# Performance work log

Measured on AMD Instinct MI355X. Metric: run time of the kernel, lower is better.

The kernel has to match this reference:

```python
import jax, jax.numpy as jnp
import numpy as np

N_NODES = 50000
N_EDGES = 800000
IN_DIM = 128
HEADS = 4
OUT_DIM = 32
NEG_SLOPE = 0.2


def setup_inputs() -> dict:
    key = jax.random.key(0)
    k_x, k_e, k_w, k_as, k_ad = jax.random.split(key, 5)
    x = jax.random.normal(k_x, (N_NODES, IN_DIM), dtype=jnp.float32)
    edge_index = jax.random.randint(k_e, (2, N_EDGES), 0, N_NODES, dtype=jnp.int32)
    # Linear(in_dim, heads*out_dim, bias=False): store as [in_dim, heads*out_dim]
    W = jax.random.normal(k_w, (IN_DIM, HEADS * OUT_DIM), dtype=jnp.float32) * 0.05
    a_src = jax.random.normal(k_as, (HEADS, OUT_DIM), dtype=jnp.float32) * 0.01
    a_dst = jax.random.normal(k_ad, (HEADS, OUT_DIM), dtype=jnp.float32) * 0.01
    return {"x": x, "edge_index": edge_index, "W": W, "a_src": a_src, "a_dst": a_dst}


def reference(x, edge_index, W, a_src, a_dst):
    N = x.shape[0]
    H, D = a_src.shape
    src, dst = edge_index[0], edge_index[1]
    h = (x @ W).reshape(N, H, D)                      # [N, H, D]
    h_src = h[src]                                    # [E, H, D] gather
    h_dst = h[dst]                                    # [E, H, D] gather
    e = jnp.einsum('ehd,hd->eh', h_src, a_src) + jnp.einsum('ehd,hd->eh', h_dst, a_dst)
    e = jax.nn.leaky_relu(e, NEG_SLOPE)               # [E, H]
    # segment softmax over dst, per head (vectorized across heads)
    m = jax.ops.segment_max(e, dst, num_segments=N)   # [N, H]
    exp = jnp.exp(e - m[dst])                         # [E, H]
    s = jax.ops.segment_sum(exp, dst, num_segments=N) # [N, H]
    alpha = exp / (s[dst] + 1e-12)                    # [E, H]
    # dropout p=0.0 -> identity
    out = jax.ops.segment_sum(alpha[:, :, None] * h_src, dst, num_segments=N)  # [N, H, D]
    return out.mean(axis=1)                           # [N, D]
```

## Files before the change

### kernel.cpp

```cpp
#include <hip/hip_runtime.h>
#include <hip/hip_bf16.h>

#define IN_DIM 128
#define HEADS 4
#define ODIM 32
#define HD (HEADS * ODIM)
#define NEG_SLOPE 0.2f

#define GM 64
#define LDK 136
#define ACCW 132

#define BIN_SHIFT 4
#define BIN_NODES 16
#define BINCAP 512
#define MAXBINS 4096
#define KE 16

#define SMEM_BYTES 52224

typedef unsigned short ushortT;
typedef __attribute__((ext_vector_type(8))) short bf16x8;
typedef __attribute__((ext_vector_type(4))) float f32x4;

static __device__ __forceinline__ ushortT f2bf(float f) {
    __hip_bfloat16 b = __float2bfloat16(f);
    return *reinterpret_cast<ushortT*>(&b);
}
static __device__ __forceinline__ float hsel(float4 v, int head) {
    return (head == 0) ? v.x : (head == 1) ? v.y : (head == 2) ? v.z : v.w;
}
static __device__ __forceinline__ float i8f(unsigned int p, int sh) {
    return (float)((int)(p << (24 - sh)) >> 24);
}

__global__ void __launch_bounds__(256) k_wconv_zero(
    const float* __restrict__ W, ushortT* __restrict__ Wt_g,
    int* __restrict__ bin_cursor, int nbins)
{
    const int idx = blockIdx.x * 256 + threadIdx.x;
    const int c = idx >> 7, k = idx & 127;
    Wt_g[c * 128 + k] = f2bf(W[k * HD + c]);
    if (idx < nbins) bin_cursor[idx] = 0;
}

__global__ void __launch_bounds__(256) k_mega(
    const float* __restrict__ x, const ushortT* __restrict__ Wt_g,
    const float* __restrict__ a_src, const float* __restrict__ a_dst,
    const int* __restrict__ src, const int* __restrict__ dst,
    unsigned char* __restrict__ h8, float* __restrict__ scales,
    float* __restrict__ s_src, float* __restrict__ s_dst,
    int* __restrict__ bin_cursor, int* __restrict__ bin_buf,
    int N, int E, int nbins, int nBinBlocks)
{
    __shared__ __align__(16) char smem[SMEM_BYTES];
    const int t = threadIdx.x;

    if ((int)blockIdx.x < nBinBlocks) {
        int* lcnt = reinterpret_cast<int*>(smem);
        int* lcur = lcnt + MAXBINS;
        for (int i = t; i < nbins; i += 256) lcnt[i] = 0;
        __syncthreads();

        const int base_e = blockIdx.x * (256 * KE);
        int b_[KE]; int p_[KE];
#pragma unroll
        for (int k = 0; k < KE; ++k) {
            const int e = base_e + k * 256 + t;
            if (e < E) {
                const int d = dst[e];
                const int s = src[e];
                b_[k] = d >> BIN_SHIFT;
                p_[k] = ((d & (BIN_NODES - 1)) << 16) | s;
                atomicAdd(&lcnt[b_[k]], 1);
            } else {
                b_[k] = -1;
            }
        }
        __syncthreads();
        for (int i = t; i < nbins; i += 256) {
            const int c = lcnt[i];
            lcur[i] = (c > 0) ? atomicAdd(&bin_cursor[i], c) : 0;
        }
        __syncthreads();
#pragma unroll
        for (int k = 0; k < KE; ++k) {
            if (b_[k] >= 0) {
                const int pos = atomicAdd(&lcur[b_[k]], 1);
                if (pos < BINCAP) bin_buf[b_[k] * BINCAP + pos] = p_[k];
            }
        }
        return;
    }

    ushortT* Xs = reinterpret_cast<ushortT*>(smem);
    ushortT* Wt = Xs + GM * LDK;

    const int n0 = ((int)blockIdx.x - nBinBlocks) * GM;

    {
#pragma unroll
        for (int it = 0; it < 8; ++it) {
            const int o = it * 2048 + t * 8;
            *reinterpret_cast<uint4*>(&Wt[(o >> 7) * LDK + (o & 127)]) =
                *reinterpret_cast<const uint4*>(&Wt_g[o]);
        }
    }
    {
        const int r  = t >> 2;
        const int k0 = (t & 3) * 32;
        const int ng = n0 + r;
        if (ng < N) {
#pragma unroll
            for (int kk = 0; kk < 32; kk += 4) {
                float4 v = *reinterpret_cast<const float4*>(
                    &x[(size_t)ng * IN_DIM + k0 + kk]);
                ushort4 u;
                u.x = f2bf(v.x); u.y = f2bf(v.y); u.z = f2bf(v.z); u.w = f2bf(v.w);
                *reinterpret_cast<ushort4*>(&Xs[r * LDK + k0 + kk]) = u;
            }
        } else {
#pragma unroll
            for (int kk = 0; kk < 32; kk += 4)
                *reinterpret_cast<ushort4*>(&Xs[r * LDK + k0 + kk]) =
                    make_ushort4(0, 0, 0, 0);
        }
    }
    __syncthreads();

    const int w  = t >> 6;
    const int l  = t & 63;
    const int lr = l & 15;
    const int lk = (l >> 4) * 8;

    f32x4 acc[8];
#pragma unroll
    for (int i = 0; i < 8; ++i) acc[i] = (f32x4)(0.f);

#pragma unroll
    for (int kt = 0; kt < 4; ++kt) {
        const bf16x8 af = *reinterpret_cast<const bf16x8*>(
            &Xs[(w * 16 + lr) * LDK + kt * 32 + lk]);
#pragma unroll
        for (int ct = 0; ct < 8; ++ct) {
            const bf16x8 bfr = *reinterpret_cast<const bf16x8*>(
                &Wt[(ct * 16 + lr) * LDK + kt * 32 + lk]);
            acc[ct] = __builtin_amdgcn_mfma_f32_16x16x32_bf16(af, bfr, acc[ct],
                                                              0, 0, 0);
        }
    }

    float aSv[8], aDv[8];
#pragma unroll
    for (int ct = 0; ct < 8; ++ct) {
        aSv[ct] = a_src[ct * 16 + lr];
        aDv[ct] = a_dst[ct * 16 + lr];
    }
    const int rbase = w * 16 + (l >> 4) * 4;

#pragma unroll
    for (int j = 0; j < 4; ++j) {
        const int ng = n0 + rbase + j;
        float ps[4] = {0.f, 0.f, 0.f, 0.f}, pd[4] = {0.f, 0.f, 0.f, 0.f};
#pragma unroll
        for (int ct = 0; ct < 8; ++ct) {
            ps[ct >> 1] = fmaf(acc[ct][j], aSv[ct], ps[ct >> 1]);
            pd[ct >> 1] = fmaf(acc[ct][j], aDv[ct], pd[ct >> 1]);
        }
#pragma unroll
        for (int o = 1; o <= 8; o <<= 1) {
#pragma unroll
            for (int hh = 0; hh < 4; ++hh) {
                ps[hh] += __shfl_xor(ps[hh], o, 64);
                pd[hh] += __shfl_xor(pd[hh], o, 64);
            }
        }
        if (lr == 0 && ng < N) {
            *reinterpret_cast<float4*>(&s_src[ng * 4]) =
                make_float4(ps[0], ps[1], ps[2], ps[3]);
            *reinterpret_cast<float4*>(&s_dst[ng * 4]) =
                make_float4(pd[0], pd[1], pd[2], pd[3]);
        }
    }

    __syncthreads();
    float* accb = reinterpret_cast<float*>(smem);

#pragma unroll
    for (int ct = 0; ct < 8; ++ct)
#pragma unroll
        for (int j = 0; j < 4; ++j)
            accb[(rbase + j) * ACCW + ct * 16 + lr] = acc[ct][j];
    __syncthreads();

    {
        const int row = t >> 2;
        const int c0  = (t & 3) * 32;
        const int ng  = n0 + row;

        float4 v[8];
        float m = 0.f;
#pragma unroll
        for (int i = 0; i < 8; ++i) {
            v[i] = *reinterpret_cast<const float4*>(&accb[row * ACCW + c0 + 4 * i]);
            m = fmaxf(m, fmaxf(fmaxf(fabsf(v[i].x), fabsf(v[i].y)),
                               fmaxf(fabsf(v[i].z), fabsf(v[i].w))));
        }
        m = fmaxf(m, __shfl_xor(m, 1, 64));
        m = fmaxf(m, __shfl_xor(m, 2, 64));

        const float inv = (m > 0.f) ? 127.f / m : 0.f;
        unsigned int p[8];
#pragma unroll
        for (int i = 0; i < 8; ++i) {
            const int q0 = __float2int_rn(v[i].x * inv);
            const int q1 = __float2int_rn(v[i].y * inv);
            const int q2 = __float2int_rn(v[i].z * inv);
            const int q3 = __float2int_rn(v[i].w * inv);
            p[i] = (q0 & 0xFF) | ((q1 & 0xFF) << 8) |
                   ((q2 & 0xFF) << 16) | ((q3 & 0xFF) << 24);
        }
        if (ng < N) {
            *reinterpret_cast<uint4*>(&h8[(size_t)ng * 128 + c0]) =
                make_uint4(p[0], p[1], p[2], p[3]);
            *reinterpret_cast<uint4*>(&h8[(size_t)ng * 128 + c0 + 16]) =
                make_uint4(p[4], p[5], p[6], p[7]);
            if ((t & 3) == 0) scales[ng] = m * (1.f / 127.f);
        }
    }
}

__global__ void __launch_bounds__(256) k_pull_binned(
    const int* __restrict__ bin_buf, const int* __restrict__ bin_cursor,
    const unsigned char* __restrict__ h8, const float* __restrict__ scales,
    const float* __restrict__ s_src, const float* __restrict__ s_dst,
    float* __restrict__ out, int N)
{
    __shared__ ushortT csr[BINCAP];
    __shared__ int cnt_s[BIN_NODES], start_s[BIN_NODES], cur_s[BIN_NODES];

    const int b = blockIdx.x;
    const int t = threadIdx.x;
    const int node0 = b << BIN_SHIFT;

    int nedge = bin_cursor[b];
    nedge = (nedge < BINCAP) ? nedge : BINCAP;

    if (t < BIN_NODES) cnt_s[t] = 0;
    __syncthreads();

    for (int i = t; i < nedge; i += 256)
        atomicAdd(&cnt_s[bin_buf[b * BINCAP + i] >> 16], 1);
    __syncthreads();

    if (t < BIN_NODES) {
        const int v = cnt_s[t];
        int inc = v;
#pragma unroll
        for (int o = 1; o < BIN_NODES; o <<= 1) {
            const int x = __shfl_up(inc, o, BIN_NODES);
            if (t >= o) inc += x;
        }
        start_s[t] = inc - v;
        cur_s[t]   = inc - v;
    }
    __syncthreads();

    for (int i = t; i < nedge; i += 256) {
        const int p = bin_buf[b * BINCAP + i];
        const int pos = atomicAdd(&cur_s[p >> 16], 1);
        csr[pos] = (ushortT)(p & 0xFFFF);
    }
    __syncthreads();

    const int wv   = t >> 6;
    const int l    = t & 63;
    const int half = l >> 5;
    const int l32  = l & 31;
    const int head = l32 >> 3;
    const int hoff = head * 8 + (l32 & 7);

    const unsigned int* hu = reinterpret_cast<const unsigned int*>(h8);
    const float4* ss4 = reinterpret_cast<const float4*>(s_src);

    for (int k = 0; k < 4; ++k) {
        const int nloc = wv * 4 + k;
        const int n = node0 + nloc;
        if (n >= N) break;

        const int st  = start_s[nloc];
        const int deg = cnt_s[nloc];
        const float4 vd4 = reinterpret_cast<const float4*>(s_dst)[n];
        const float vd = hsel(vd4, head);

        float den = 0.f;
        float a0 = 0.f, a1 = 0.f, a2 = 0.f, a3 = 0.f;

        const int count = (deg - half + 1) >> 1;
        for (int j = 0; j < count; j += 4) {
            const int i0 = st + 2 * j + half;
            const bool v1 = (j + 1) < count;
            const bool v2 = (j + 2) < count;
            const bool v3 = (j + 3) < count;
            const int s0 = csr[i0];
            const int s1 = v1 ? csr[i0 + 2] : s0;
            const int s2 = v2 ? csr[i0 + 4] : s0;
            const int s3 = v3 ? csr[i0 + 6] : s0;

            const float4 w0 = ss4[s0];
            const float4 w1 = ss4[s1];
            const float4 w2 = ss4[s2];
            const float4 w3 = ss4[s3];
            const float sc0 = scales[s0];
            const float sc1 = scales[s1];
            const float sc2 = scales[s2];
            const float sc3 = scales[s3];
            const unsigned int q0 = hu[(size_t)s0 * 32 + hoff];
            const unsigned int q1 = hu[(size_t)s1 * 32 + hoff];
            const unsigned int q2 = hu[(size_t)s2 * 32 + hoff];
            const unsigned int q3 = hu[(size_t)s3 * 32 + hoff];

            float e0 = hsel(w0, head) + vd;
            float e1 = hsel(w1, head) + vd;
            float e2 = hsel(w2, head) + vd;
            float e3 = hsel(w3, head) + vd;
            e0 = (e0 > 0.f) ? e0 : NEG_SLOPE * e0;
            e1 = (e1 > 0.f) ? e1 : NEG_SLOPE * e1;
            e2 = (e2 > 0.f) ? e2 : NEG_SLOPE * e2;
            e3 = (e3 > 0.f) ? e3 : NEG_SLOPE * e3;
            const float x0 = __expf(e0);
            const float x1 = v1 ? __expf(e1) : 0.f;
            const float x2 = v2 ? __expf(e2) : 0.f;
            const float x3 = v3 ? __expf(e3) : 0.f;

            den += (x0 + x1) + (x2 + x3);
            const float ws0 = x0 * sc0;
            const float ws1 = x1 * sc1;
            const float ws2 = x2 * sc2;
            const float ws3 = x3 * sc3;

            a0 = fmaf(ws0, i8f(q0, 0), a0);  a1 = fmaf(ws0, i8f(q0, 8), a1);
            a2 = fmaf(ws0, i8f(q0, 16), a2); a3 = fmaf(ws0, i8f(q0, 24), a3);
            a0 = fmaf(ws1, i8f(q1, 0), a0);  a1 = fmaf(ws1, i8f(q1, 8), a1);
            a2 = fmaf(ws1, i8f(q1, 16), a2); a3 = fmaf(ws1, i8f(q1, 24), a3);
            a0 = fmaf(ws2, i8f(q2, 0), a0);  a1 = fmaf(ws2, i8f(q2, 8), a1);
            a2 = fmaf(ws2, i8f(q2, 16), a2); a3 = fmaf(ws2, i8f(q2, 24), a3);
            a0 = fmaf(ws3, i8f(q3, 0), a0);  a1 = fmaf(ws3, i8f(q3, 8), a1);
            a2 = fmaf(ws3, i8f(q3, 16), a2); a3 = fmaf(ws3, i8f(q3, 24), a3);
        }

        a0 += __shfl_xor(a0, 32, 64);
        a1 += __shfl_xor(a1, 32, 64);
        a2 += __shfl_xor(a2, 32, 64);
        a3 += __shfl_xor(a3, 32, 64);
        den += __shfl_xor(den, 32, 64);

        const float inv = 1.f / (den + 1e-12f);
        a0 *= inv; a1 *= inv; a2 *= inv; a3 *= inv;

        a0 += __shfl_xor(a0, 8, 64);  a0 += __shfl_xor(a0, 16, 64);
        a1 += __shfl_xor(a1, 8, 64);  a1 += __shfl_xor(a1, 16, 64);
        a2 += __shfl_xor(a2, 8, 64);  a2 += __shfl_xor(a2, 16, 64);
        a3 += __shfl_xor(a3, 8, 64);  a3 += __shfl_xor(a3, 16, 64);

        if (l < 8) {
            float4 o4 = make_float4(0.25f * a0, 0.25f * a1, 0.25f * a2, 0.25f * a3);
            *reinterpret_cast<float4*>(&out[(size_t)n * ODIM + l * 4]) = o4;
        }
    }
}

extern "C" void kernel_launch(void* const* d_in, const int* in_sizes, int n_in,
                              void* d_out, int out_size, void* d_ws, size_t ws_size,
                              hipStream_t stream)
{
    const float* x      = (const float*)d_in[0];
    const int*   eidx   = (const int*)d_in[1];
    const float* W      = (const float*)d_in[2];
    const float* a_src  = (const float*)d_in[3];
    const float* a_dst  = (const float*)d_in[4];
    float* out = (float*)d_out;

    const int N = in_sizes[0] / IN_DIM;
    const int E = in_sizes[1] / 2;
    const int* src = eidx;
    const int* dst = eidx + E;

    const int nbins = (N + BIN_NODES - 1) >> BIN_SHIFT;

    char* wsp = (char*)d_ws;
    unsigned char* h8 = (unsigned char*)wsp; wsp += (size_t)N * 128;
    float* scales   = (float*)wsp;    wsp += (size_t)N * sizeof(float);
    float* s_src    = (float*)wsp;    wsp += (size_t)N * HEADS * sizeof(float);
    float* s_dst    = (float*)wsp;    wsp += (size_t)N * HEADS * sizeof(float);
    ushortT* Wt_g   = (ushortT*)wsp;  wsp += (size_t)128 * 128 * sizeof(ushortT);
    int* bin_buf    = (int*)wsp;      wsp += (size_t)nbins * BINCAP * sizeof(int);
    int* bin_cursor = (int*)wsp;      wsp += (size_t)nbins * sizeof(int);

    k_wconv_zero<<<64, 256, 0, stream>>>(W, Wt_g, bin_cursor, nbins);

    {
        const int epb = 256 * KE;
        const int nBinBlocks  = (E + epb - 1) / epb;
        const int nGemmBlocks = (N + GM - 1) / GM;
        k_mega<<<nBinBlocks + nGemmBlocks, 256, 0, stream>>>(
            x, Wt_g, a_src, a_dst, src, dst,
            h8, scales, s_src, s_dst, bin_cursor, bin_buf,
            N, E, nbins, nBinBlocks);
    }

    k_pull_binned<<<nbins, 256, 0, stream>>>(bin_buf, bin_cursor, h8, scales,
                                             s_src, s_dst, out, N);
}
```

Baseline: 72.19 us.

## Halve bin size for more pull blocks and move attention scores into quantize pass

The destination-bin size drops from 16 to 8 nodes, with per-bin capacity and the max bin count adjusted to match. Each wave in the pull kernel now handles 2 nodes instead of 4, so the kernel launches twice as many blocks to improve occupancy and load balance. Separately, the per-head source and destination attention dot products are no longer computed with MFMA-register shuffle reductions. They are now computed from the staged accumulator tile in the quantization pass, where each thread owns one head-row, which removes the cross-lane shuffles. The cost is more vector loads of a_src and a_dst per thread, and a smaller bin capacity that could overflow for high-degree bins.

```diff
diff --git a/kernel.cpp b/kernel.cpp
--- a/kernel.cpp
+++ b/kernel.cpp
@@ -11,10 +11,10 @@
 #define LDK 136
 #define ACCW 132
 
-#define BIN_SHIFT 4
-#define BIN_NODES 16
-#define BINCAP 512
-#define MAXBINS 4096
+#define BIN_SHIFT 3
+#define BIN_NODES 8
+#define BINCAP 256
+#define MAXBINS 6400
 #define KE 16
 
 #define SMEM_BYTES 52224
@@ -150,39 +150,7 @@
         }
     }
 
-    float aSv[8], aDv[8];
-#pragma unroll
-    for (int ct = 0; ct < 8; ++ct) {
-        aSv[ct] = a_src[ct * 16 + lr];
-        aDv[ct] = a_dst[ct * 16 + lr];
-    }
     const int rbase = w * 16 + (l >> 4) * 4;
-
-#pragma unroll
-    for (int j = 0; j < 4; ++j) {
-        const int ng = n0 + rbase + j;
-        float ps[4] = {0.f, 0.f, 0.f, 0.f}, pd[4] = {0.f, 0.f, 0.f, 0.f};
-#pragma unroll
-        for (int ct = 0; ct < 8; ++ct) {
-            ps[ct >> 1] = fmaf(acc[ct][j], aSv[ct], ps[ct >> 1]);
-            pd[ct >> 1] = fmaf(acc[ct][j], aDv[ct], pd[ct >> 1]);
-        }
-#pragma unroll
-        for (int o = 1; o <= 8; o <<= 1) {
-#pragma unroll
-            for (int hh = 0; hh < 4; ++hh) {
-                ps[hh] += __shfl_xor(ps[hh], o, 64);
-                pd[hh] += __shfl_xor(pd[hh], o, 64);
-            }
-        }
-        if (lr == 0 && ng < N) {
-            *reinterpret_cast<float4*>(&s_src[ng * 4]) =
-                make_float4(ps[0], ps[1], ps[2], ps[3]);
-            *reinterpret_cast<float4*>(&s_dst[ng * 4]) =
-                make_float4(pd[0], pd[1], pd[2], pd[3]);
-        }
-    }
-
     __syncthreads();
     float* accb = reinterpret_cast<float*>(smem);
 
@@ -194,17 +162,23 @@
     __syncthreads();
 
     {
-        const int row = t >> 2;
-        const int c0  = (t & 3) * 32;
-        const int ng  = n0 + row;
+        const int row  = t >> 2;
+        const int head = t & 3;
+        const int c0   = head * 32;
+        const int ng   = n0 + row;
 
         float4 v[8];
         float m = 0.f;
+        float ps = 0.f, pd = 0.f;
 #pragma unroll
         for (int i = 0; i < 8; ++i) {
             v[i] = *reinterpret_cast<const float4*>(&accb[row * ACCW + c0 + 4 * i]);
             m = fmaxf(m, fmaxf(fmaxf(fabsf(v[i].x), fabsf(v[i].y)),
                                fmaxf(fabsf(v[i].z), fabsf(v[i].w))));
+            const float4 as = *reinterpret_cast<const float4*>(&a_src[c0 + 4 * i]);
+            const float4 ad = *reinterpret_cast<const float4*>(&a_dst[c0 + 4 * i]);
+            ps += v[i].x * as.x + v[i].y * as.y + v[i].z * as.z + v[i].w * as.w;
+            pd += v[i].x * ad.x + v[i].y * ad.y + v[i].z * ad.z + v[i].w * ad.w;
         }
         m = fmaxf(m, __shfl_xor(m, 1, 64));
         m = fmaxf(m, __shfl_xor(m, 2, 64));
@@ -225,7 +199,9 @@
                 make_uint4(p[0], p[1], p[2], p[3]);
             *reinterpret_cast<uint4*>(&h8[(size_t)ng * 128 + c0 + 16]) =
                 make_uint4(p[4], p[5], p[6], p[7]);
-            if ((t & 3) == 0) scales[ng] = m * (1.f / 127.f);
+            s_src[ng * 4 + head] = ps;
+            s_dst[ng * 4 + head] = pd;
+            if (head == 0) scales[ng] = m * (1.f / 127.f);
         }
     }
 }
@@ -283,8 +259,8 @@
     const unsigned int* hu = reinterpret_cast<const unsigned int*>(h8);
     const float4* ss4 = reinterpret_cast<const float4*>(s_src);
 
-    for (int k = 0; k < 4; ++k) {
-        const int nloc = wv * 4 + k;
+    for (int k = 0; k < 2; ++k) {
+        const int nloc = wv * 2 + k;
         const int n = node0 + nloc;
         if (n >= N) break;
 
```

Result: slower. 77.68 us (+7.6%).
